# Performance work log

Measured on AMD Instinct MI355X. Metric: run time of the kernel, lower is better.

## Reference

```python
import jax, jax.numpy as jnp
import numpy as np
import math

B, NP, PL, CIN = 32, 1024, 16, 8
C = PL * CIN          # channels = 128
D = 512               # d_model
H = 8                 # n_heads
DH = D // H           # 64
DFF = 2048
E, TOPK = 4, 2
M = int(DH * math.log(DH))  # 266 performer random features


def _ortho_proj(m, d, rng):
    # gaussian-orthogonal random features, rows rescaled by gaussian norms (FAVOR+, scaling=0)
    blocks = []
    for _ in range(m // d + 1):
        q, _ = np.linalg.qr(rng.normal(size=(d, d)))
        blocks.append(q.T)
    mat = np.concatenate(blocks, 0)[:m]
    mult = np.linalg.norm(rng.normal(size=(m, d)), axis=1)
    return jnp.asarray((mat * mult[:, None]).astype(np.float32))


def setup_inputs() -> dict:
    key = jax.random.key(0)
    ks = jax.random.split(key, 16)
    rng = np.random.default_rng(0)
    s = lambda k, sh, fan: (jax.random.normal(k, sh, jnp.float32) / np.sqrt(fan))
    return {
        "x": jax.random.normal(ks[0], (B, NP, PL, CIN), jnp.float32),
        "emb_w": s(ks[1], (D, C), C),
        "wq": s(ks[2], (D, D), D), "bq": jnp.zeros((D,), jnp.float32),
        "wk": s(ks[3], (D, D), D), "bk": jnp.zeros((D,), jnp.float32),
        "wv": s(ks[4], (D, D), D), "bv": jnp.zeros((D,), jnp.float32),
        "wo": s(ks[5], (D, D), D), "bo": jnp.zeros((D,), jnp.float32),
        "proj": _ortho_proj(M, DH, rng),
        "ln2_g": jnp.ones((D,), jnp.float32), "ln2_b": jnp.zeros((D,), jnp.float32),
        "ln3_g": jnp.ones((D,), jnp.float32), "ln3_b": jnp.zeros((D,), jnp.float32),
        "gate_w": s(ks[6], (E, D), D), "gate_b": jnp.zeros((E,), jnp.float32),
        "w1": s(ks[7], (E, D, DFF), D), "b1": jnp.zeros((E, DFF), jnp.float32),
        "w2": s(ks[8], (E, DFF, D), DFF), "b2": jnp.zeros((E, D), jnp.float32),
    }


def _ln(x, g, b):
    mu = jnp.mean(x, -1, keepdims=True)
    var = jnp.var(x, -1, keepdims=True)
    return (x - mu) / jnp.sqrt(var + 1e-5) * g + b


def _phi(data, proj, is_query):
    # FAVOR+ softmax kernel feature map
    dh = data.shape[-1]
    m = proj.shape[0]
    dn = dh ** -0.25
    dash = jnp.einsum('...nd,md->...nm', data * dn, proj)
    diag = jnp.sum(jnp.square(data), -1, keepdims=True) * (0.5 * dn * dn)
    stab = jnp.max(dash, -1, keepdims=True) if is_query else jnp.max(dash)
    return (m ** -0.5) * (jnp.exp(dash - diag - stab) + 1e-4)


def reference(x, emb_w, wq, bq, wk, bk, wv, bv, wo, bo, proj,
              ln2_g, ln2_b, ln3_g, ln3_b, gate_w, gate_b, w1, b1, w2, b2):
    b, n = x.shape[0], x.shape[1]
    xe = x.reshape(b, n, -1) @ emb_w.T          # [b, n, D] (bias-free embedding)
    xe = xe[:, None]                            # [b, 1, n, D]
    # ---- Performer self-attention ----
    heads = lambda t: t.reshape(b, 1, n, H, DH).transpose(0, 1, 3, 2, 4)  # [b,1,h,n,dh]
    q = heads(xe @ wq.T + bq)
    k = heads(xe @ wk.T + bk)
    v = heads(xe @ wv.T + bv)
    qp = _phi(q, proj, True)                    # [b,1,h,n,m]
    kp = _phi(k, proj, False)
    ctx = jnp.einsum('...nm,...nd->...md', kp, v)           # [b,1,h,m,dh]
    den = jnp.einsum('...nm,...m->...n', qp, kp.sum(-2))    # [b,1,h,n]
    attn = jnp.einsum('...nm,...md->...nd', qp, ctx) / den[..., None]
    attn = attn.transpose(0, 1, 3, 2, 4).reshape(b, 1, n, D) @ wo.T + bo
    h1 = _ln(xe + attn, ln2_g, ln2_b)
    # ---- SparseMoE feed-forward (top-2 of 4 experts) ----
    t = h1.reshape(-1, D)                       # [T, D], T = b*n
    logits = t @ gate_w.T + gate_b              # [T, E]
    topv, topi = jax.lax.top_k(logits, TOPK)
    gwt = jax.nn.softmax(topv, -1)              # softmax over selected experts
    wfull = (jax.nn.one_hot(topi, E, dtype=t.dtype) * gwt[..., None]).sum(1)  # [T, E]
    hmid = jax.nn.relu(jnp.einsum('td,edf->etf', t, w1) + b1[:, None])        # [E, T, DFF]
    y = jnp.einsum('etf,efd->etd', hmid, w2) + b2[:, None]                    # [E, T, D]
    moe = jnp.einsum('te,etd->td', wfull, y).reshape(b, 1, n, D)
    return _ln(h1 + moe, ln3_g, ln3_b)          # dropout = identity in eval
```

## Files before the change

### kernel.cpp

```cpp
#include <hip/hip_runtime.h>
#include <math.h>

#define NBATCH 32
#define NPOS   1024
#define NTOK   32768
#define DMODEL 512
#define NHEAD  8
#define DHD    64
#define NROWS  262144
#define MMR    266
#define NDFF   2048
#define NEXP   4
#define CIN    128

#define DNSC   0.35355339059327373f
#define RSM    0.06131393394849658f
#define NEG_INF -3.0e38f

typedef _Float16 half8 __attribute__((ext_vector_type(8)));
typedef float    f32x4 __attribute__((ext_vector_type(4)));

static const size_t F_BUF1 = 0;
static const size_t F_CTX  = 16777216;
static const size_t F_KSUM = 21135360;
static const size_t F_PART = 21203456;
static const size_t F_STAB = 21205504;
static const size_t F_EFF  = 21205520;
static const size_t F_CNTI = 21402128;
static const size_t F_TOKI = 21402144;
static const size_t F_GWF  = 21533216;
static const size_t F_END  = 21664288;

__global__ __launch_bounds__(256) void fallback_zero_kernel(float* __restrict__ out) {
  out[(size_t)blockIdx.x * 256 + threadIdx.x] = 0.f;
}

__global__ __launch_bounds__(256) void zero_range_kernel(float* __restrict__ p, int n) {
  int i = blockIdx.x * 256 + threadIdx.x;
  if (i < n) p[i] = 0.f;
}

__global__ __launch_bounds__(128) void effmat_kernel(
    const float* __restrict__ wq, const float* __restrict__ wk, const float* __restrict__ wv,
    const float* __restrict__ emb, float* __restrict__ eff)
{
  __shared__ float wrow[512];
  const int bid = blockIdx.x;
  const int mat = bid >> 9;
  const int n   = bid & 511;
  const float* W = (mat == 0) ? wq : ((mat == 1) ? wk : wv);
  const int tid = threadIdx.x;
  for (int i = tid; i < 512; i += 128) wrow[i] = W[n * 512 + i];
  __syncthreads();
  float acc = 0.f;
  for (int d = 0; d < 512; ++d) acc += wrow[d] * emb[d * CIN + tid];
  eff[mat * 65536 + n * CIN + tid] = acc;
}

__device__ __forceinline__ void stage_proj(float* pj, const float* __restrict__ proj, int tid) {
  for (int idx = tid; idx < 272 * 68; idx += 256) pj[idx] = 0.f;
  __syncthreads();
  for (int idx = tid; idx < MMR * 64; idx += 256) {
    int m = idx >> 6, d = idx & 63;
    pj[m * 68 + d] = proj[idx];
  }
}

__global__ __launch_bounds__(256) void gemm_nt_kernel(
    const float* __restrict__ A, const float* __restrict__ W, int K,
    const float* __restrict__ A2, const float* __restrict__ W2, int K2,
    const float* __restrict__ bias, float* __restrict__ C, int N, int ncb)
{
  __shared__ float As[32][64];
  __shared__ float Ws[32][64];
  const int tid  = threadIdx.x;
  const int bx   = blockIdx.x % ncb;
  const int by   = blockIdx.x / ncb;
  const int row0 = by * 64, col0 = bx * 64;
  const int tx   = tid & 15, ty = tid >> 4;
  const int lr   = tid >> 3;
  const int lk   = (tid & 7) * 4;
  float acc[4][4] = {};
  for (int pass = 0; pass < 2; ++pass) {
    const float* Ap = pass ? A2 : A;
    const float* Wp = pass ? W2 : W;
    const int    Kp = pass ? K2 : K;
    if (!Ap) continue;
    for (int k0 = 0; k0 < Kp; k0 += 32) {
      __syncthreads();
#pragma unroll
      for (int rr = 0; rr < 2; ++rr) {
        const int r = lr + rr * 32;
        float4 a4 = *(const float4*)&Ap[(size_t)(row0 + r) * Kp + k0 + lk];
        As[lk + 0][r] = a4.x; As[lk + 1][r] = a4.y; As[lk + 2][r] = a4.z; As[lk + 3][r] = a4.w;
        float4 w4 = *(const float4*)&Wp[(size_t)(col0 + r) * Kp + k0 + lk];
        Ws[lk + 0][r] = w4.x; Ws[lk + 1][r] = w4.y; Ws[lk + 2][r] = w4.z; Ws[lk + 3][r] = w4.w;
      }
      __syncthreads();
#pragma unroll
      for (int kk = 0; kk < 32; ++kk) {
        float4 av = *(const float4*)&As[kk][ty * 4];
        float4 wv = *(const float4*)&Ws[kk][tx * 4];
        acc[0][0] += av.x * wv.x; acc[0][1] += av.x * wv.y; acc[0][2] += av.x * wv.z; acc[0][3] += av.x * wv.w;
        acc[1][0] += av.y * wv.x; acc[1][1] += av.y * wv.y; acc[1][2] += av.y * wv.z; acc[1][3] += av.y * wv.w;
        acc[2][0] += av.z * wv.x; acc[2][1] += av.z * wv.y; acc[2][2] += av.z * wv.z; acc[2][3] += av.z * wv.w;
        acc[3][0] += av.w * wv.x; acc[3][1] += av.w * wv.y; acc[3][2] += av.w * wv.z; acc[3][3] += av.w * wv.w;
      }
    }
  }
#pragma unroll
  for (int i = 0; i < 4; ++i) {
    const int row = row0 + ty * 4 + i;
    const int col = col0 + tx * 4;
    float4 o = make_float4(acc[i][0], acc[i][1], acc[i][2], acc[i][3]);
    if (bias) {
      float4 b4 = *(const float4*)&bias[col];
      o.x += b4.x; o.y += b4.y; o.z += b4.z; o.w += b4.w;
    }
    *(float4*)&C[(size_t)row * N + col] = o;
  }
}

__global__ __launch_bounds__(256) void kdash_max_kernel(
    const float* __restrict__ Kbuf, const float* __restrict__ proj, float* __restrict__ partial)
{
  __shared__ float pj[272 * 68];
  __shared__ float kl[32 * 68];
  __shared__ float red[256];
  const int tid = threadIdx.x;
  stage_proj(pj, proj, tid);
  const int i8 = tid >> 3, ml = tid & 7, mb = ml * 34;
  const size_t rid0 = (size_t)blockIdx.x * 128;
  float mx = NEG_INF;
  for (int ch = 0; ch < 4; ++ch) {
    __syncthreads();
    for (int idx = tid; idx < 2048; idx += 256) {
      int r = idx >> 6, dd = idx & 63;
      kl[r * 68 + dd] = Kbuf[(rid0 + ch * 32 + r) * 64 + dd] * DNSC;
    }
    __syncthreads();
    float dacc[34];
#pragma unroll
    for (int j = 0; j < 34; ++j) dacc[j] = 0.f;
    for (int d0 = 0; d0 < 64; d0 += 4) {
      float4 k4 = *(const float4*)&kl[i8 * 68 + d0];
#pragma unroll
      for (int j = 0; j < 34; ++j) {
        float4 p4 = *(const float4*)&pj[(mb + j) * 68 + d0];
        dacc[j] += k4.x * p4.x + k4.y * p4.y + k4.z * p4.z + k4.w * p4.w;
      }
    }
#pragma unroll
    for (int j = 0; j < 34; ++j) {
      int m = mb + j;
      mx = fmaxf(mx, (m < MMR) ? dacc[j] : NEG_INF);
    }
  }
  red[tid] = mx;
  __syncthreads();
  for (int st = 128; st > 0; st >>= 1) {
    if (tid < st) red[tid] = fmaxf(red[tid], red[tid + st]);
    __syncthreads();
  }
  if (tid == 0) partial[blockIdx.x] = red[0];
}

__global__ __launch_bounds__(256) void reduce_max_kernel(
    const float* __restrict__ part, float* __restrict__ stab, int n)
{
  __shared__ float red[256];
  float m = NEG_INF;
  for (int i = threadIdx.x; i < n; i += 256) m = fmaxf(m, part[i]);
  red[threadIdx.x] = m;
  __syncthreads();
  for (int st = 128; st > 0; st >>= 1) {
    if (threadIdx.x < st) red[threadIdx.x] = fmaxf(red[threadIdx.x], red[threadIdx.x + st]);
    __syncthreads();
  }
  if (threadIdx.x == 0) stab[0] = red[0];
}

__global__ __launch_bounds__(256) void ctx_kernel(
    const float* __restrict__ Kbuf, const float* __restrict__ Vbuf,
    const float* __restrict__ proj, const float* __restrict__ stabp,
    float* __restrict__ ctxg, float* __restrict__ ksumg)
{
  __shared__ float pj[272 * 68];
  __shared__ float kl[32 * 68];
  __shared__ float vl[32 * 68];
  __shared__ float kp[32 * 272];
  __shared__ float ks[272];
  const int tid = threadIdx.x;
  const int bh = blockIdx.x & 255;
  const int chunk = blockIdx.x >> 8;
  const int b = bh >> 3, h = bh & 7;
  const float stab = stabp[0];
  stage_proj(pj, proj, tid);
  for (int m = tid; m < 272; m += 256) ks[m] = 0.f;
  const int d = tid & 63, mg = tid >> 6;
  const int i8 = tid >> 3, ml = tid & 7, mb = ml * 34;
  float acc[68];
#pragma unroll
  for (int jj = 0; jj < 68; ++jj) acc[jj] = 0.f;
  for (int n0 = chunk * 256; n0 < chunk * 256 + 256; n0 += 32) {
    __syncthreads();
    for (int idx = tid; idx < 2048; idx += 256) {
      int r = idx >> 6, dd = idx & 63;
      size_t g = ((size_t)(b * NPOS + n0 + r)) * DMODEL + h * DHD + dd;
      kl[r * 68 + dd] = Kbuf[g] * DNSC;
      vl[r * 68 + dd] = Vbuf[g];
    }
    __syncthreads();
    float dacc[34];
#pragma unroll
    for (int j = 0; j < 34; ++j) dacc[j] = 0.f;
    float diag = 0.f;
    for (int d0 = 0; d0 < 64; d0 += 4) {
      float4 k4 = *(const float4*)&kl[i8 * 68 + d0];
      diag += k4.x * k4.x + k4.y * k4.y + k4.z * k4.z + k4.w * k4.w;
#pragma unroll
      for (int j = 0; j < 34; ++j) {
        float4 p4 = *(const float4*)&pj[(mb + j) * 68 + d0];
        dacc[j] += k4.x * p4.x + k4.y * p4.y + k4.z * p4.z + k4.w * p4.w;
      }
    }
    diag *= 0.5f;
#pragma unroll
    for (int j = 0; j < 34; ++j) {
      int m = mb + j;
      if (m < MMR) kp[i8 * 272 + m] = RSM * (expf(dacc[j] - diag - stab) + 1e-4f);
    }
    if (ml < 6) kp[i8 * 272 + MMR + ml] = 0.f;
    __syncthreads();
    for (int m = tid; m < MMR; m += 256) {
      float s = 0.f;
#pragma unroll 8
      for (int i = 0; i < 32; ++i) s += kp[i * 272 + m];
      ks[m] += s;
    }
    for (int i = 0; i < 32; ++i) {
      const float vv = vl[i * 68 + d];
      const float* kr = &kp[i * 272 + mg * 68];
#pragma unroll
      for (int jj = 0; jj < 17; ++jj) {
        float4 k4 = *(const float4*)&kr[jj * 4];
        acc[4 * jj + 0] += k4.x * vv;
        acc[4 * jj + 1] += k4.y * vv;
        acc[4 * jj + 2] += k4.z * vv;
        acc[4 * jj + 3] += k4.w * vv;
      }
    }
  }
  const size_t cb = (size_t)bh * MMR * DHD;
#pragma unroll
  for (int jj = 0; jj < 68; ++jj) {
    int m = mg * 68 + jj;
    if (m < MMR) atomicAdd(&ctxg[cb + (size_t)m * 64 + d], acc[jj]);
  }
  for (int m = tid; m < MMR; m += 256) atomicAdd(&ksumg[bh * MMR + m], ks[m]);
}

__global__ __launch_bounds__(256) void attn_kernel(
    const float* __restrict__ Qbuf, const float* __restrict__ ctxg,
    const float* __restrict__ ksumg, const float* __restrict__ proj,
    float* __restrict__ attnb)
{
  __shared__ float pj[272 * 68];
  __shared__ float ql[32 * 68];
  __shared__ float qp[32 * 272];
  __shared__ float ks[272];
  __shared__ float den_s[32];
  const int tid = threadIdx.x;
  const int bh = blockIdx.x >> 5;
  const int nc = blockIdx.x & 31;
  const int b = bh >> 3, h = bh & 7;
  const int n0 = nc * 32;
  stage_proj(pj, proj, tid);
  for (int m = tid; m < 272; m += 256) ks[m] = (m < MMR) ? ksumg[bh * MMR + m] : 0.f;
  for (int idx = tid; idx < 2048; idx += 256) {
    int r = idx >> 6, dd = idx & 63;
    ql[r * 68 + dd] = Qbuf[((size_t)(b * NPOS + n0 + r)) * DMODEL + h * DHD + dd] * DNSC;
  }
  __syncthreads();
  const int i8 = tid >> 3, ml = tid & 7, mb = ml * 34;
  float dacc[34];
#pragma unroll
  for (int j = 0; j < 34; ++j) dacc[j] = 0.f;
  float diag = 0.f;
  for (int d0 = 0; d0 < 64; d0 += 4) {
    float4 k4 = *(const float4*)&ql[i8 * 68 + d0];
    diag += k4.x * k4.x + k4.y * k4.y + k4.z * k4.z + k4.w * k4.w;
#pragma unroll
    for (int j = 0; j < 34; ++j) {
      float4 p4 = *(const float4*)&pj[(mb + j) * 68 + d0];
      dacc[j] += k4.x * p4.x + k4.y * p4.y + k4.z * p4.z + k4.w * p4.w;
    }
  }
  diag *= 0.5f;
  float mx = NEG_INF;
#pragma unroll
  for (int j = 0; j < 34; ++j) {
    int m = mb + j;
    mx = fmaxf(mx, (m < MMR) ? dacc[j] : NEG_INF);
  }
#pragma unroll
  for (int off = 1; off < 8; off <<= 1) mx = fmaxf(mx, __shfl_xor(mx, off));
  float dp = 0.f;
#pragma unroll
  for (int j = 0; j < 34; ++j) {
    int m = mb + j;
    if (m < MMR) {
      float v = RSM * (expf(dacc[j] - diag - mx) + 1e-4f);
      qp[i8 * 272 + m] = v;
      dp += v * ks[m];
    }
  }
  if (ml < 6) qp[i8 * 272 + MMR + ml] = 0.f;
#pragma unroll
  for (int off = 1; off < 8; off <<= 1) dp += __shfl_xor(dp, off);
  if (ml == 0) den_s[i8] = dp;
  __syncthreads();
  const int lane = tid & 63, wid = tid >> 6;
  float acc[8];
#pragma unroll
  for (int t = 0; t < 8; ++t) acc[t] = 0.f;
  const float* cb = ctxg + (size_t)bh * MMR * DHD + lane;
  for (int m0 = 0; m0 < 264; m0 += 4) {
    float c0 = cb[(size_t)(m0 + 0) * 64];
    float c1 = cb[(size_t)(m0 + 1) * 64];
    float c2 = cb[(size_t)(m0 + 2) * 64];
    float c3 = cb[(size_t)(m0 + 3) * 64];
#pragma unroll
    for (int t = 0; t < 8; ++t) {
      float4 q4 = *(const float4*)&qp[(wid + 4 * t) * 272 + m0];
      acc[t] += q4.x * c0 + q4.y * c1 + q4.z * c2 + q4.w * c3;
    }
  }
  {
    float c0 = cb[264 * 64], c1 = cb[265 * 64];
#pragma unroll
    for (int t = 0; t < 8; ++t)
      acc[t] += qp[(wid + 4 * t) * 272 + 264] * c0 + qp[(wid + 4 * t) * 272 + 265] * c1;
  }
#pragma unroll
  for (int t = 0; t < 8; ++t) {
    int r = wid + 4 * t;
    size_t o = ((size_t)(b * NPOS + n0 + r)) * DMODEL + h * DHD + lane;
    attnb[o] = acc[t] / den_s[r];
  }
}

__global__ __launch_bounds__(256) void ln_kernel(
    const float* __restrict__ in, const float* __restrict__ g, const float* __restrict__ bb,
    float* __restrict__ out, float* __restrict__ out2)
{
  const int row = blockIdx.x, tid = threadIdx.x;
  float2 x = *(const float2*)&in[(size_t)row * DMODEL + tid * 2];
  float s = x.x + x.y, sq = x.x * x.x + x.y * x.y;
#pragma unroll
  for (int off = 32; off > 0; off >>= 1) {
    s += __shfl_down(s, off);
    sq += __shfl_down(sq, off);
  }
  __shared__ float ps[4], pq[4];
  __shared__ float smu, srv;
  const int wv = tid >> 6, ln = tid & 63;
  if (ln == 0) { ps[wv] = s; pq[wv] = sq; }
  __syncthreads();
  if (tid == 0) {
    float S = ps[0] + ps[1] + ps[2] + ps[3];
    float Q = pq[0] + pq[1] + pq[2] + pq[3];
    float mu = S / 512.f;
    float var = Q / 512.f - mu * mu;
    smu = mu;
    srv = 1.0f / sqrtf(var + 1e-5f);
  }
  __syncthreads();
  const float mu = smu, rv = srv;
  const int c = tid * 2;
  float y0 = (x.x - mu) * rv * g[c] + bb[c];
  float y1 = (x.y - mu) * rv * g[c + 1] + bb[c + 1];
  out[(size_t)row * DMODEL + c] = y0;
  out[(size_t)row * DMODEL + c + 1] = y1;
  if (out2) {
    out2[(size_t)row * DMODEL + c] = y0;
    out2[(size_t)row * DMODEL + c + 1] = y1;
  }
}

__global__ __launch_bounds__(64) void zero_cnt_kernel(int* __restrict__ cnt)
{
  if (threadIdx.x < NEXP) cnt[threadIdx.x] = 0;
}

__global__ __launch_bounds__(256) void gate_kernel(
    const float* __restrict__ h1, const float* __restrict__ gw, const float* __restrict__ gb,
    int* __restrict__ cnt, int* __restrict__ toks, float* __restrict__ gws)
{
  const int wv = threadIdx.x >> 6, ln = threadIdx.x & 63;
  const int tok = blockIdx.x * 4 + wv;
  const float* hr = h1 + (size_t)tok * DMODEL;
  float p0 = 0, p1 = 0, p2 = 0, p3 = 0;
#pragma unroll
  for (int k = 0; k < 8; ++k) {
    float xv = hr[ln + 64 * k];
    p0 += xv * gw[0 * DMODEL + ln + 64 * k];
    p1 += xv * gw[1 * DMODEL + ln + 64 * k];
    p2 += xv * gw[2 * DMODEL + ln + 64 * k];
    p3 += xv * gw[3 * DMODEL + ln + 64 * k];
  }
#pragma unroll
  for (int off = 32; off > 0; off >>= 1) {
    p0 += __shfl_down(p0, off);
    p1 += __shfl_down(p1, off);
    p2 += __shfl_down(p2, off);
    p3 += __shfl_down(p3, off);
  }
  if (ln == 0) {
    p0 += gb[0]; p1 += gb[1]; p2 += gb[2]; p3 += gb[3];
    int i0 = 0; float v0 = p0;
    if (p1 > v0) { v0 = p1; i0 = 1; }
    if (p2 > v0) { v0 = p2; i0 = 2; }
    if (p3 > v0) { v0 = p3; i0 = 3; }
    int i1 = -1; float v1 = NEG_INF;
    if (i0 != 0 && p0 > v1) { v1 = p0; i1 = 0; }
    if (i0 != 1 && p1 > v1) { v1 = p1; i1 = 1; }
    if (i0 != 2 && p2 > v1) { v1 = p2; i1 = 2; }
    if (i0 != 3 && p3 > v1) { v1 = p3; i1 = 3; }
    float e = expf(v1 - v0);
    float w0 = 1.f / (1.f + e);
    float w1 = e / (1.f + e);
    int pos0 = atomicAdd(&cnt[i0], 1);
    toks[i0 * NTOK + pos0] = tok;
    gws[i0 * NTOK + pos0] = w0;
    int pos1 = atomicAdd(&cnt[i1], 1);
    toks[i1 * NTOK + pos1] = tok;
    gws[i1 * NTOK + pos1] = w1;
  }
}

__global__ __launch_bounds__(256) void transpose_f16_kernel(
    const float* __restrict__ in, _Float16* __restrict__ outp, int R, int C)
{
  __shared__ float tl[32][33];
  const int bid = blockIdx.x;
  const int e  = bid >> 10;
  const int t2 = bid & 1023;
  const int tC = C >> 5;
  const int r0 = (t2 / tC) << 5;
  const int c0 = (t2 % tC) << 5;
  const float* ine  = in   + (size_t)e * R * C;
  _Float16*    oute = outp + (size_t)e * R * C;
  const int ci = threadIdx.x & 31, ri = threadIdx.x >> 5;
#pragma unroll
  for (int i = 0; i < 4; ++i)
    tl[ri + i * 8][ci] = ine[(size_t)(r0 + ri + i * 8) * C + c0 + ci];
  __syncthreads();
  const int rr = threadIdx.x & 31, cc = threadIdx.x >> 5;
#pragma unroll
  for (int i = 0; i < 4; ++i)
    oute[(size_t)(c0 + cc + i * 8) * R + r0 + rr] = (_Float16)tl[rr][cc + i * 8];
}

__global__ __launch_bounds__(512) void moe_mfma_kernel(
    const float* __restrict__ h1, const _Float16* __restrict__ w1t, const float* __restrict__ b1,
    const _Float16* __restrict__ w2t, const float* __restrict__ b2,
    const int* __restrict__ cnt, const int* __restrict__ toks, const float* __restrict__ gws,
    float* __restrict__ Z)
{
  __shared__ _Float16 t_lds[64 * 520];
  __shared__ _Float16 hm[64 * 264];
  __shared__ int   tk_s[64];
  __shared__ float gw_s[64];
  const int tid = threadIdx.x;
  const int e = blockIdx.x >> 10;
  const int tile = blockIdx.x & 1023;
  const int cn = cnt[e];
  if (tile * 64 >= cn) return;
  if (tid < 64) {
    int idx = tile * 64 + tid;
    if (idx < cn) { tk_s[tid] = toks[e * NTOK + idx]; gw_s[tid] = gws[e * NTOK + idx]; }
    else          { tk_s[tid] = -1;                   gw_s[tid] = 0.f; }
  }
  __syncthreads();
  for (int it = tid; it < 64 * 128; it += 512) {
    int r = it >> 7, c4 = (it & 127) * 4;
    int tk = tk_s[r];
    float4 v = make_float4(0.f, 0.f, 0.f, 0.f);
    if (tk >= 0) v = *(const float4*)&h1[(size_t)tk * DMODEL + c4];
    _Float16* p = &t_lds[r * 520 + c4];
    p[0] = (_Float16)v.x; p[1] = (_Float16)v.y; p[2] = (_Float16)v.z; p[3] = (_Float16)v.w;
  }
  __syncthreads();

  const int w = tid >> 6, l = tid & 63;
  const int lr = l & 15, lg = l >> 4;
  const _Float16* w1e = w1t + (size_t)e * NDFF * DMODEL;
  const _Float16* w2e = w2t + (size_t)e * DMODEL * NDFF;
  const float* b1e = b1 + e * NDFF;

  f32x4 acc2[4][4];
#pragma unroll
  for (int mt = 0; mt < 4; ++mt)
#pragma unroll
    for (int nt = 0; nt < 4; ++nt) acc2[mt][nt] = (f32x4){0.f, 0.f, 0.f, 0.f};

  for (int fc = 0; fc < 8; ++fc) {
    f32x4 acc1[4][2];
#pragma unroll
    for (int mt = 0; mt < 4; ++mt)
#pragma unroll
      for (int nt1 = 0; nt1 < 2; ++nt1) acc1[mt][nt1] = (f32x4){0.f, 0.f, 0.f, 0.f};
#pragma unroll
    for (int ks = 0; ks < 16; ++ks) {
      half8 am[4];
#pragma unroll
      for (int mt = 0; mt < 4; ++mt)
        am[mt] = *(const half8*)&t_lds[(mt * 16 + lr) * 520 + ks * 32 + lg * 8];
#pragma unroll
      for (int nt1 = 0; nt1 < 2; ++nt1) {
        half8 bfr = *(const half8*)&w1e[(size_t)(fc * 256 + w * 32 + nt1 * 16 + lr) * DMODEL + ks * 32 + lg * 8];
#pragma unroll
        for (int mt = 0; mt < 4; ++mt)
          acc1[mt][nt1] = __builtin_amdgcn_mfma_f32_16x16x32_f16(am[mt], bfr, acc1[mt][nt1], 0, 0, 0);
      }
    }
#pragma unroll
    for (int nt1 = 0; nt1 < 2; ++nt1) {
      float b1v = b1e[fc * 256 + w * 32 + nt1 * 16 + lr];
#pragma unroll
      for (int mt = 0; mt < 4; ++mt)
#pragma unroll
        for (int r = 0; r < 4; ++r)
          hm[(mt * 16 + lg * 4 + r) * 264 + w * 32 + nt1 * 16 + lr] =
              (_Float16)fmaxf(acc1[mt][nt1][r] + b1v, 0.f);
    }
    __syncthreads();
#pragma unroll
    for (int ks2 = 0; ks2 < 8; ++ks2) {
      half8 am[4];
#pragma unroll
      for (int mt = 0; mt < 4; ++mt)
        am[mt] = *(const half8*)&hm[(mt * 16 + lr) * 264 + ks2 * 32 + lg * 8];
#pragma unroll
      for (int nt = 0; nt < 4; ++nt) {
        half8 bfr = *(const half8*)&w2e[(size_t)(w * 64 + nt * 16 + lr) * NDFF + fc * 256 + ks2 * 32 + lg * 8];
#pragma unroll
        for (int mt = 0; mt < 4; ++mt)
          acc2[mt][nt] = __builtin_amdgcn_mfma_f32_16x16x32_f16(am[mt], bfr, acc2[mt][nt], 0, 0, 0);
      }
    }
    __syncthreads();
  }

  const float* b2e = b2 + e * DMODEL;
#pragma unroll
  for (int nt = 0; nt < 4; ++nt) {
    float b2v = b2e[w * 64 + nt * 16 + lr];
#pragma unroll
    for (int mt = 0; mt < 4; ++mt) {
#pragma unroll
      for (int r = 0; r < 4; ++r) {
        int row = mt * 16 + lg * 4 + r;
        int tk = tk_s[row];
        if (tk >= 0)
          atomicAdd(&Z[(size_t)tk * DMODEL + w * 64 + nt * 16 + lr],
                    (acc2[mt][nt][r] + b2v) * gw_s[row]);
      }
    }
  }
}

extern "C" void kernel_launch(void* const* d_in, const int* in_sizes, int n_in,
                              void* d_out, int out_size, void* d_ws, size_t ws_size,
                              hipStream_t stream) {
  const float* x     = (const float*)d_in[0];
  const float* emb_w = (const float*)d_in[1];
  const float* wq    = (const float*)d_in[2];
  const float* bq    = (const float*)d_in[3];
  const float* wk    = (const float*)d_in[4];
  const float* bk    = (const float*)d_in[5];
  const float* wv    = (const float*)d_in[6];
  const float* bv    = (const float*)d_in[7];
  const float* wo    = (const float*)d_in[8];
  const float* bo    = (const float*)d_in[9];
  const float* proj  = (const float*)d_in[10];
  const float* ln2g  = (const float*)d_in[11];
  const float* ln2b  = (const float*)d_in[12];
  const float* ln3g  = (const float*)d_in[13];
  const float* ln3b  = (const float*)d_in[14];
  const float* gatew = (const float*)d_in[15];
  const float* gateb = (const float*)d_in[16];
  const float* w1    = (const float*)d_in[17];
  const float* b1    = (const float*)d_in[18];
  const float* w2    = (const float*)d_in[19];
  const float* b2    = (const float*)d_in[20];
  float* out = (float*)d_out;
  float* ws  = (float*)d_ws;

  if (ws_size < F_END * sizeof(float)) {
    fallback_zero_kernel<<<NTOK * 2, 256, 0, stream>>>(out);
    return;
  }

  float* BUF1 = ws + F_BUF1;
  float* BUF2 = out;
  int*   cnt  = (int*)(ws + F_CNTI);
  int*   toks = (int*)(ws + F_TOKI);
  float* gwf  = ws + F_GWF;
  _Float16* w1t = (_Float16*)(ws + F_CTX);
  _Float16* w2t = w1t + (size_t)NEXP * NDFF * DMODEL;

  zero_cnt_kernel<<<1, 64, 0, stream>>>(cnt);
  zero_range_kernel<<<17292, 256, 0, stream>>>(ws + F_CTX, 4358144 + 68096);
  effmat_kernel<<<1536, 128, 0, stream>>>(wq, wk, wv, emb_w, ws + F_EFF);
  gemm_nt_kernel<<<4096, 256, 0, stream>>>(x, ws + F_EFF + 65536, CIN, nullptr, nullptr, 0, bk, BUF1, DMODEL, 8);
  gemm_nt_kernel<<<4096, 256, 0, stream>>>(x, ws + F_EFF + 131072, CIN, nullptr, nullptr, 0, bv, BUF2, DMODEL, 8);
  kdash_max_kernel<<<2048, 256, 0, stream>>>(BUF1, proj, ws + F_PART);
  reduce_max_kernel<<<1, 256, 0, stream>>>(ws + F_PART, ws + F_STAB, 2048);
  ctx_kernel<<<1024, 256, 0, stream>>>(BUF1, BUF2, proj, ws + F_STAB, ws + F_CTX, ws + F_KSUM);
  gemm_nt_kernel<<<4096, 256, 0, stream>>>(x, ws + F_EFF, CIN, nullptr, nullptr, 0, bq, BUF1, DMODEL, 8);
  attn_kernel<<<8192, 256, 0, stream>>>(BUF1, ws + F_CTX, ws + F_KSUM, proj, BUF2);
  transpose_f16_kernel<<<4096, 256, 0, stream>>>(w1, w1t, DMODEL, NDFF);
  transpose_f16_kernel<<<4096, 256, 0, stream>>>(w2, w2t, NDFF, DMODEL);
  gemm_nt_kernel<<<4096, 256, 0, stream>>>(BUF2, wo, DMODEL, x, emb_w, CIN, bo, BUF1, DMODEL, 8);
  ln_kernel<<<NTOK, 256, 0, stream>>>(BUF1, ln2g, ln2b, BUF2, BUF1);
  gate_kernel<<<8192, 256, 0, stream>>>(BUF2, gatew, gateb, cnt, toks, gwf);
  moe_mfma_kernel<<<4096, 512, 0, stream>>>(BUF2, w1t, b1, w2t, b2, cnt, toks, gwf, BUF1);
  ln_kernel<<<NTOK, 256, 0, stream>>>(BUF1, ln3g, ln3b, out, nullptr);
}
```

Measured before the change: 4.495 ms.

## Restructure performer feature kernels with packed proj layout and wider blocks

Adds a one-time pack of the random-feature projection into a d-major, 17-feature-grouped layout. The k-max, ctx and attention kernels now run as 1024-thread blocks that split the 64-dim dot product across lane quarters and reduce with shuffles. The ctx kernel now uses one block per batch-head over the full sequence and writes its results directly, which removes the global atomics and the workspace zeroing kernel. Feature values kp/qp are stored in LDS as fp16 to cut shared-memory footprint and bandwidth, at some cost in precision. Fewer ctx blocks (256) may reduce occupancy, and LDS use per block grows.

```diff
diff --git a/kernel.cpp b/kernel.cpp
--- a/kernel.cpp
+++ b/kernel.cpp
@@ -18,6 +18,7 @@
 #define NEG_INF -3.0e38f
 
 typedef _Float16 half8 __attribute__((ext_vector_type(8)));
+typedef _Float16 half4 __attribute__((ext_vector_type(4)));
 typedef float    f32x4 __attribute__((ext_vector_type(4)));
 
 static const size_t F_BUF1 = 0;
@@ -29,15 +30,29 @@
 static const size_t F_CNTI = 21402128;
 static const size_t F_TOKI = 21402144;
 static const size_t F_GWF  = 21533216;
-static const size_t F_END  = 21664288;
+static const size_t F_PJT  = 21664288;
+static const size_t F_END  = 21684768;
+
+#define DASH17(da, q) \
+  da[0]+=q*pA.x; da[1]+=q*pA.y; da[2]+=q*pA.z; da[3]+=q*pA.w; \
+  da[4]+=q*pB.x; da[5]+=q*pB.y; da[6]+=q*pB.z; da[7]+=q*pB.w; \
+  da[8]+=q*pC.x; da[9]+=q*pC.y; da[10]+=q*pC.z; da[11]+=q*pC.w; \
+  da[12]+=q*pD.x; da[13]+=q*pD.y; da[14]+=q*pD.z; da[15]+=q*pD.w; \
+  da[16]+=q*pE;
 
 __global__ __launch_bounds__(256) void fallback_zero_kernel(float* __restrict__ out) {
   out[(size_t)blockIdx.x * 256 + threadIdx.x] = 0.f;
 }
 
-__global__ __launch_bounds__(256) void zero_range_kernel(float* __restrict__ p, int n) {
-  int i = blockIdx.x * 256 + threadIdx.x;
-  if (i < n) p[i] = 0.f;
+__global__ __launch_bounds__(256) void proj_pack_kernel(
+    const float* __restrict__ proj, float* __restrict__ projT)
+{
+  int idx = blockIdx.x * 256 + threadIdx.x;
+  if (idx >= 20480) return;
+  int d = idx / 320, rem = idx % 320;
+  int g = rem / 20, j = rem % 20;
+  int m = g * 17 + j;
+  projT[idx] = (j < 17 && m < MMR) ? proj[m * 64 + d] : 0.f;
 }
 
 __global__ __launch_bounds__(128) void effmat_kernel(
@@ -55,15 +70,6 @@
   float acc = 0.f;
   for (int d = 0; d < 512; ++d) acc += wrow[d] * emb[d * CIN + tid];
   eff[mat * 65536 + n * CIN + tid] = acc;
-}
-
-__device__ __forceinline__ void stage_proj(float* pj, const float* __restrict__ proj, int tid) {
-  for (int idx = tid; idx < 272 * 68; idx += 256) pj[idx] = 0.f;
-  __syncthreads();
-  for (int idx = tid; idx < MMR * 64; idx += 256) {
-    int m = idx >> 6, d = idx & 63;
-    pj[m * 68 + d] = proj[idx];
-  }
 }
 
 __global__ __launch_bounds__(256) void gemm_nt_kernel(
@@ -121,44 +127,53 @@
   }
 }
 
-__global__ __launch_bounds__(256) void kdash_max_kernel(
-    const float* __restrict__ Kbuf, const float* __restrict__ proj, float* __restrict__ partial)
-{
-  __shared__ float pj[272 * 68];
+__global__ __launch_bounds__(1024) void kdash_max_kernel(
+    const float* __restrict__ Kbuf, const float* __restrict__ projT, float* __restrict__ partial)
+{
+  __shared__ float pjG[20480];
   __shared__ float kl[32 * 68];
-  __shared__ float red[256];
+  __shared__ float red[1024];
   const int tid = threadIdx.x;
-  stage_proj(pj, proj, tid);
-  const int i8 = tid >> 3, ml = tid & 7, mb = ml * 34;
-  const size_t rid0 = (size_t)blockIdx.x * 128;
-  float mx = NEG_INF;
-  for (int ch = 0; ch < 4; ++ch) {
-    __syncthreads();
-    for (int idx = tid; idx < 2048; idx += 256) {
+  for (int i = tid; i < 20480; i += 1024) pjG[i] = projT[i];
+  const int w = tid >> 6, l = tid & 63;
+  const int ml = l & 15, ds = l >> 4;
+  const int dbase = ds * 16;
+  const int r0 = 2 * w;
+  float mxl = NEG_INF;
+  for (int t = 0; t < 16; ++t) {
+    __syncthreads();
+    for (int idx = tid; idx < 2048; idx += 1024) {
       int r = idx >> 6, dd = idx & 63;
-      kl[r * 68 + dd] = Kbuf[(rid0 + ch * 32 + r) * 64 + dd] * DNSC;
-    }
-    __syncthreads();
-    float dacc[34];
-#pragma unroll
-    for (int j = 0; j < 34; ++j) dacc[j] = 0.f;
-    for (int d0 = 0; d0 < 64; d0 += 4) {
-      float4 k4 = *(const float4*)&kl[i8 * 68 + d0];
-#pragma unroll
-      for (int j = 0; j < 34; ++j) {
-        float4 p4 = *(const float4*)&pj[(mb + j) * 68 + d0];
-        dacc[j] += k4.x * p4.x + k4.y * p4.y + k4.z * p4.z + k4.w * p4.w;
-      }
-    }
-#pragma unroll
-    for (int j = 0; j < 34; ++j) {
-      int m = mb + j;
-      mx = fmaxf(mx, (m < MMR) ? dacc[j] : NEG_INF);
-    }
-  }
-  red[tid] = mx;
-  __syncthreads();
-  for (int st = 128; st > 0; st >>= 1) {
+      kl[r * 68 + dd] = Kbuf[((size_t)blockIdx.x * 512 + t * 32 + r) * 64 + dd] * DNSC;
+    }
+    __syncthreads();
+    float da0[17], da1[17];
+#pragma unroll
+    for (int j = 0; j < 17; ++j) { da0[j] = 0.f; da1[j] = 0.f; }
+    for (int dd = 0; dd < 16; ++dd) {
+      int d = dbase + dd;
+      float q0 = kl[r0 * 68 + d], q1 = kl[r0 * 68 + 68 + d];
+      const float* pr = &pjG[d * 320 + ml * 20];
+      float4 pA = *(const float4*)pr, pB = *(const float4*)(pr + 4),
+             pC = *(const float4*)(pr + 8), pD = *(const float4*)(pr + 12);
+      float pE = pr[16];
+      DASH17(da0, q0)
+      DASH17(da1, q1)
+    }
+#pragma unroll
+    for (int j = 0; j < 17; ++j) {
+      da0[j] += __shfl_xor(da0[j], 16); da0[j] += __shfl_xor(da0[j], 32);
+      da1[j] += __shfl_xor(da1[j], 16); da1[j] += __shfl_xor(da1[j], 32);
+    }
+#pragma unroll
+    for (int j = 0; j < 17; ++j) {
+      int m = ml * 17 + j;
+      if (m < MMR) { mxl = fmaxf(mxl, da0[j]); mxl = fmaxf(mxl, da1[j]); }
+    }
+  }
+  red[tid] = mxl;
+  __syncthreads();
+  for (int st = 512; st > 0; st >>= 1) {
     if (tid < st) red[tid] = fmaxf(red[tid], red[tid + st]);
     __syncthreads();
   }
@@ -180,173 +195,208 @@
   if (threadIdx.x == 0) stab[0] = red[0];
 }
 
-__global__ __launch_bounds__(256) void ctx_kernel(
+__global__ __launch_bounds__(1024) void ctx_kernel(
     const float* __restrict__ Kbuf, const float* __restrict__ Vbuf,
-    const float* __restrict__ proj, const float* __restrict__ stabp,
+    const float* __restrict__ projT, const float* __restrict__ stabp,
     float* __restrict__ ctxg, float* __restrict__ ksumg)
 {
-  __shared__ float pj[272 * 68];
+  __shared__ float pjG[20480];
   __shared__ float kl[32 * 68];
   __shared__ float vl[32 * 68];
-  __shared__ float kp[32 * 272];
+  __shared__ _Float16 kp16[32 * 320];
   __shared__ float ks[272];
   const int tid = threadIdx.x;
-  const int bh = blockIdx.x & 255;
-  const int chunk = blockIdx.x >> 8;
+  const int bh = blockIdx.x;
   const int b = bh >> 3, h = bh & 7;
   const float stab = stabp[0];
-  stage_proj(pj, proj, tid);
-  for (int m = tid; m < 272; m += 256) ks[m] = 0.f;
+  for (int i = tid; i < 20480; i += 1024) pjG[i] = projT[i];
+  if (tid < 272) ks[tid] = 0.f;
+  const int w = tid >> 6, l = tid & 63;
+  const int ml = l & 15, ds = l >> 4;
+  const int dbase = ds * 16;
+  const int r0 = 2 * w;
+  const int jh = ds >> 1, rsel = ds & 1;
   const int d = tid & 63, mg = tid >> 6;
-  const int i8 = tid >> 3, ml = tid & 7, mb = ml * 34;
-  float acc[68];
-#pragma unroll
-  for (int jj = 0; jj < 68; ++jj) acc[jj] = 0.f;
-  for (int n0 = chunk * 256; n0 < chunk * 256 + 256; n0 += 32) {
-    __syncthreads();
-    for (int idx = tid; idx < 2048; idx += 256) {
+  const int ksm = tid >> 1, ksih = tid & 1;
+  const int ksg = ksm / 17, ksj = ksm - ksg * 17;
+  float acc[17];
+#pragma unroll
+  for (int j = 0; j < 17; ++j) acc[j] = 0.f;
+
+  for (int t = 0; t < 32; ++t) {
+    __syncthreads();
+    for (int idx = tid; idx < 2048; idx += 1024) {
       int r = idx >> 6, dd = idx & 63;
-      size_t g = ((size_t)(b * NPOS + n0 + r)) * DMODEL + h * DHD + dd;
+      size_t g = ((size_t)(b * NPOS + t * 32 + r)) * DMODEL + h * DHD + dd;
       kl[r * 68 + dd] = Kbuf[g] * DNSC;
       vl[r * 68 + dd] = Vbuf[g];
     }
     __syncthreads();
-    float dacc[34];
-#pragma unroll
-    for (int j = 0; j < 34; ++j) dacc[j] = 0.f;
-    float diag = 0.f;
-    for (int d0 = 0; d0 < 64; d0 += 4) {
-      float4 k4 = *(const float4*)&kl[i8 * 68 + d0];
-      diag += k4.x * k4.x + k4.y * k4.y + k4.z * k4.z + k4.w * k4.w;
-#pragma unroll
-      for (int j = 0; j < 34; ++j) {
-        float4 p4 = *(const float4*)&pj[(mb + j) * 68 + d0];
-        dacc[j] += k4.x * p4.x + k4.y * p4.y + k4.z * p4.z + k4.w * p4.w;
+    float da0[17], da1[17]; float dg0 = 0.f, dg1 = 0.f;
+#pragma unroll
+    for (int j = 0; j < 17; ++j) { da0[j] = 0.f; da1[j] = 0.f; }
+    for (int dd = 0; dd < 16; ++dd) {
+      int dq = dbase + dd;
+      float q0 = kl[r0 * 68 + dq], q1 = kl[r0 * 68 + 68 + dq];
+      const float* pr = &pjG[dq * 320 + ml * 20];
+      float4 pA = *(const float4*)pr, pB = *(const float4*)(pr + 4),
+             pC = *(const float4*)(pr + 8), pD = *(const float4*)(pr + 12);
+      float pE = pr[16];
+      dg0 += q0 * q0; dg1 += q1 * q1;
+      DASH17(da0, q0)
+      DASH17(da1, q1)
+    }
+#pragma unroll
+    for (int j = 0; j < 17; ++j) {
+      da0[j] += __shfl_xor(da0[j], 16); da0[j] += __shfl_xor(da0[j], 32);
+      da1[j] += __shfl_xor(da1[j], 16); da1[j] += __shfl_xor(da1[j], 32);
+    }
+    dg0 += __shfl_xor(dg0, 16); dg0 += __shfl_xor(dg0, 32);
+    dg1 += __shfl_xor(dg1, 16); dg1 += __shfl_xor(dg1, 32);
+    float dgx = rsel ? dg1 : dg0;
+    const int irow = r0 + rsel;
+#pragma unroll
+    for (int k = 0; k < 9; ++k) {
+      int j = 2 * k + jh;
+      if (j < 17) {
+        int m = ml * 17 + j;
+        float dv = rsel ? da1[j] : da0[j];
+        float v = 0.f;
+        if (m < MMR) v = RSM * (expf(dv - 0.5f * dgx - stab) + 1e-4f);
+        kp16[irow * 320 + ml * 20 + j] = (_Float16)v;
       }
     }
-    diag *= 0.5f;
-#pragma unroll
-    for (int j = 0; j < 34; ++j) {
-      int m = mb + j;
-      if (m < MMR) kp[i8 * 272 + m] = RSM * (expf(dacc[j] - diag - stab) + 1e-4f);
-    }
-    if (ml < 6) kp[i8 * 272 + MMR + ml] = 0.f;
-    __syncthreads();
-    for (int m = tid; m < MMR; m += 256) {
+    __syncthreads();
+    if (tid < 544) {
       float s = 0.f;
-#pragma unroll 8
-      for (int i = 0; i < 32; ++i) s += kp[i * 272 + m];
-      ks[m] += s;
+      const _Float16* kb = &kp16[ksih * 16 * 320 + ksg * 20 + ksj];
+#pragma unroll
+      for (int i = 0; i < 16; ++i) s += (float)kb[i * 320];
+      s += __shfl_xor(s, 1);
+      if (ksih == 0) ks[ksm] += s;
     }
     for (int i = 0; i < 32; ++i) {
-      const float vv = vl[i * 68 + d];
-      const float* kr = &kp[i * 272 + mg * 68];
-#pragma unroll
-      for (int jj = 0; jj < 17; ++jj) {
-        float4 k4 = *(const float4*)&kr[jj * 4];
-        acc[4 * jj + 0] += k4.x * vv;
-        acc[4 * jj + 1] += k4.y * vv;
-        acc[4 * jj + 2] += k4.z * vv;
-        acc[4 * jj + 3] += k4.w * vv;
-      }
-    }
-  }
+      float vv = vl[i * 68 + d];
+      const _Float16* kr = &kp16[i * 320 + mg * 20];
+      half4 k0 = *(const half4*)kr;
+      half4 k1 = *(const half4*)(kr + 4);
+      half4 k2 = *(const half4*)(kr + 8);
+      half4 k3 = *(const half4*)(kr + 12);
+      float kE = (float)kr[16];
+      acc[0] += (float)k0.x * vv; acc[1] += (float)k0.y * vv; acc[2] += (float)k0.z * vv; acc[3] += (float)k0.w * vv;
+      acc[4] += (float)k1.x * vv; acc[5] += (float)k1.y * vv; acc[6] += (float)k1.z * vv; acc[7] += (float)k1.w * vv;
+      acc[8] += (float)k2.x * vv; acc[9] += (float)k2.y * vv; acc[10] += (float)k2.z * vv; acc[11] += (float)k2.w * vv;
+      acc[12] += (float)k3.x * vv; acc[13] += (float)k3.y * vv; acc[14] += (float)k3.z * vv; acc[15] += (float)k3.w * vv;
+      acc[16] += kE * vv;
+    }
+  }
+  __syncthreads();
   const size_t cb = (size_t)bh * MMR * DHD;
 #pragma unroll
-  for (int jj = 0; jj < 68; ++jj) {
-    int m = mg * 68 + jj;
-    if (m < MMR) atomicAdd(&ctxg[cb + (size_t)m * 64 + d], acc[jj]);
-  }
-  for (int m = tid; m < MMR; m += 256) atomicAdd(&ksumg[bh * MMR + m], ks[m]);
-}
-
-__global__ __launch_bounds__(256) void attn_kernel(
+  for (int j = 0; j < 17; ++j) {
+    int m = mg * 17 + j;
+    if (m < MMR) ctxg[cb + (size_t)m * 64 + d] = acc[j];
+  }
+  if (tid < MMR) ksumg[bh * MMR + tid] = ks[tid];
+}
+
+__global__ __launch_bounds__(1024) void attn_kernel(
     const float* __restrict__ Qbuf, const float* __restrict__ ctxg,
-    const float* __restrict__ ksumg, const float* __restrict__ proj,
+    const float* __restrict__ ksumg, const float* __restrict__ projT,
     float* __restrict__ attnb)
 {
-  __shared__ float pj[272 * 68];
-  __shared__ float ql[32 * 68];
-  __shared__ float qp[32 * 272];
+  __shared__ float pjG[20480];
+  __shared__ float ql[64 * 68];
+  __shared__ _Float16 qp16[64 * 272];
   __shared__ float ks[272];
-  __shared__ float den_s[32];
+  __shared__ float den_s[64];
   const int tid = threadIdx.x;
-  const int bh = blockIdx.x >> 5;
-  const int nc = blockIdx.x & 31;
+  const int bh = blockIdx.x >> 4;
+  const int n0 = (blockIdx.x & 15) * 64;
   const int b = bh >> 3, h = bh & 7;
-  const int n0 = nc * 32;
-  stage_proj(pj, proj, tid);
-  for (int m = tid; m < 272; m += 256) ks[m] = (m < MMR) ? ksumg[bh * MMR + m] : 0.f;
-  for (int idx = tid; idx < 2048; idx += 256) {
+  for (int i = tid; i < 20480; i += 1024) pjG[i] = projT[i];
+  if (tid < 272) ks[tid] = (tid < MMR) ? ksumg[bh * MMR + tid] : 0.f;
+  for (int idx = tid; idx < 4096; idx += 1024) {
     int r = idx >> 6, dd = idx & 63;
     ql[r * 68 + dd] = Qbuf[((size_t)(b * NPOS + n0 + r)) * DMODEL + h * DHD + dd] * DNSC;
   }
   __syncthreads();
-  const int i8 = tid >> 3, ml = tid & 7, mb = ml * 34;
-  float dacc[34];
-#pragma unroll
-  for (int j = 0; j < 34; ++j) dacc[j] = 0.f;
-  float diag = 0.f;
-  for (int d0 = 0; d0 < 64; d0 += 4) {
-    float4 k4 = *(const float4*)&ql[i8 * 68 + d0];
-    diag += k4.x * k4.x + k4.y * k4.y + k4.z * k4.z + k4.w * k4.w;
-#pragma unroll
-    for (int j = 0; j < 34; ++j) {
-      float4 p4 = *(const float4*)&pj[(mb + j) * 68 + d0];
-      dacc[j] += k4.x * p4.x + k4.y * p4.y + k4.z * p4.z + k4.w * p4.w;
-    }
-  }
-  diag *= 0.5f;
-  float mx = NEG_INF;
-#pragma unroll
-  for (int j = 0; j < 34; ++j) {
-    int m = mb + j;
-    mx = fmaxf(mx, (m < MMR) ? dacc[j] : NEG_INF);
-  }
-#pragma unroll
-  for (int off = 1; off < 8; off <<= 1) mx = fmaxf(mx, __shfl_xor(mx, off));
-  float dp = 0.f;
-#pragma unroll
-  for (int j = 0; j < 34; ++j) {
-    int m = mb + j;
-    if (m < MMR) {
-      float v = RSM * (expf(dacc[j] - diag - mx) + 1e-4f);
-      qp[i8 * 272 + m] = v;
-      dp += v * ks[m];
-    }
-  }
-  if (ml < 6) qp[i8 * 272 + MMR + ml] = 0.f;
-#pragma unroll
-  for (int off = 1; off < 8; off <<= 1) dp += __shfl_xor(dp, off);
-  if (ml == 0) den_s[i8] = dp;
-  __syncthreads();
-  const int lane = tid & 63, wid = tid >> 6;
-  float acc[8];
-#pragma unroll
-  for (int t = 0; t < 8; ++t) acc[t] = 0.f;
+  const int w = tid >> 6, l = tid & 63;
+  const int ml = l & 15, ds = l >> 4;
+  const int dbase = ds * 16;
+  const int jh = ds >> 1, rsel = ds & 1;
+  for (int s = 0; s < 2; ++s) {
+    const int r0 = s * 32 + 2 * w;
+    float da0[17], da1[17]; float dg0 = 0.f, dg1 = 0.f;
+#pragma unroll
+    for (int j = 0; j < 17; ++j) { da0[j] = 0.f; da1[j] = 0.f; }
+    for (int dd = 0; dd < 16; ++dd) {
+      int dq = dbase + dd;
+      float q0 = ql[r0 * 68 + dq], q1 = ql[r0 * 68 + 68 + dq];
+      const float* pr = &pjG[dq * 320 + ml * 20];
+      float4 pA = *(const float4*)pr, pB = *(const float4*)(pr + 4),
+             pC = *(const float4*)(pr + 8), pD = *(const float4*)(pr + 12);
+      float pE = pr[16];
+      dg0 += q0 * q0; dg1 += q1 * q1;
+      DASH17(da0, q0)
+      DASH17(da1, q1)
+    }
+#pragma unroll
+    for (int j = 0; j < 17; ++j) {
+      da0[j] += __shfl_xor(da0[j], 16); da0[j] += __shfl_xor(da0[j], 32);
+      da1[j] += __shfl_xor(da1[j], 16); da1[j] += __shfl_xor(da1[j], 32);
+    }
+    dg0 += __shfl_xor(dg0, 16); dg0 += __shfl_xor(dg0, 32);
+    dg1 += __shfl_xor(dg1, 16); dg1 += __shfl_xor(dg1, 32);
+    float mx0 = NEG_INF, mx1 = NEG_INF;
+#pragma unroll
+    for (int j = 0; j < 17; ++j) {
+      int m = ml * 17 + j;
+      if (m < MMR) { mx0 = fmaxf(mx0, da0[j]); mx1 = fmaxf(mx1, da1[j]); }
+    }
+#pragma unroll
+    for (int off = 1; off < 16; off <<= 1) {
+      mx0 = fmaxf(mx0, __shfl_xor(mx0, off));
+      mx1 = fmaxf(mx1, __shfl_xor(mx1, off));
+    }
+    float dgx = rsel ? dg1 : dg0;
+    float mxx = rsel ? mx1 : mx0;
+    const int row = r0 + rsel;
+    float dp = 0.f;
+#pragma unroll
+    for (int k = 0; k < 9; ++k) {
+      int j = 2 * k + jh;
+      if (j < 17) {
+        int m = ml * 17 + j;
+        float dv = rsel ? da1[j] : da0[j];
+        float v = 0.f;
+        if (m < MMR) { v = RSM * (expf(dv - 0.5f * dgx - mxx) + 1e-4f); dp += v * ks[m]; }
+        qp16[row * 272 + m] = (_Float16)v;
+      }
+    }
+    dp += __shfl_xor(dp, 1); dp += __shfl_xor(dp, 2); dp += __shfl_xor(dp, 4);
+    dp += __shfl_xor(dp, 8); dp += __shfl_xor(dp, 32);
+    if ((l & 47) == 0) den_s[row] = dp;
+  }
+  __syncthreads();
+  const int wg = tid >> 6, lane = tid & 63;
+  float acc[4] = {0.f, 0.f, 0.f, 0.f};
   const float* cb = ctxg + (size_t)bh * MMR * DHD + lane;
-  for (int m0 = 0; m0 < 264; m0 += 4) {
+  for (int m0 = 0; m0 < 272; m0 += 4) {
     float c0 = cb[(size_t)(m0 + 0) * 64];
     float c1 = cb[(size_t)(m0 + 1) * 64];
     float c2 = cb[(size_t)(m0 + 2) * 64];
     float c3 = cb[(size_t)(m0 + 3) * 64];
 #pragma unroll
-    for (int t = 0; t < 8; ++t) {
-      float4 q4 = *(const float4*)&qp[(wid + 4 * t) * 272 + m0];
-      acc[t] += q4.x * c0 + q4.y * c1 + q4.z * c2 + q4.w * c3;
-    }
-  }
-  {
-    float c0 = cb[264 * 64], c1 = cb[265 * 64];
-#pragma unroll
-    for (int t = 0; t < 8; ++t)
-      acc[t] += qp[(wid + 4 * t) * 272 + 264] * c0 + qp[(wid + 4 * t) * 272 + 265] * c1;
-  }
-#pragma unroll
-  for (int t = 0; t < 8; ++t) {
-    int r = wid + 4 * t;
-    size_t o = ((size_t)(b * NPOS + n0 + r)) * DMODEL + h * DHD + lane;
-    attnb[o] = acc[t] / den_s[r];
+    for (int tt = 0; tt < 4; ++tt) {
+      half4 q4 = *(const half4*)&qp16[(wg * 4 + tt) * 272 + m0];
+      acc[tt] += (float)q4.x * c0 + (float)q4.y * c1 + (float)q4.z * c2 + (float)q4.w * c3;
+    }
+  }
+#pragma unroll
+  for (int tt = 0; tt < 4; ++tt) {
+    int r = wg * 4 + tt;
+    attnb[((size_t)(b * NPOS + n0 + r)) * DMODEL + h * DHD + lane] = acc[tt] / den_s[r];
   }
 }
 
@@ -612,15 +662,15 @@
   _Float16* w2t = w1t + (size_t)NEXP * NDFF * DMODEL;
 
   zero_cnt_kernel<<<1, 64, 0, stream>>>(cnt);
-  zero_range_kernel<<<17292, 256, 0, stream>>>(ws + F_CTX, 4358144 + 68096);
+  proj_pack_kernel<<<80, 256, 0, stream>>>(proj, ws + F_PJT);
   effmat_kernel<<<1536, 128, 0, stream>>>(wq, wk, wv, emb_w, ws + F_EFF);
   gemm_nt_kernel<<<4096, 256, 0, stream>>>(x, ws + F_EFF + 65536, CIN, nullptr, nullptr, 0, bk, BUF1, DMODEL, 8);
   gemm_nt_kernel<<<4096, 256, 0, stream>>>(x, ws + F_EFF + 131072, CIN, nullptr, nullptr, 0, bv, BUF2, DMODEL, 8);
-  kdash_max_kernel<<<2048, 256, 0, stream>>>(BUF1, proj, ws + F_PART);
-  reduce_max_kernel<<<1, 256, 0, stream>>>(ws + F_PART, ws + F_STAB, 2048);
-  ctx_kernel<<<1024, 256, 0, stream>>>(BUF1, BUF2, proj, ws + F_STAB, ws + F_CTX, ws + F_KSUM);
+  kdash_max_kernel<<<512, 1024, 0, stream>>>(BUF1, ws + F_PJT, ws + F_PART);
+  reduce_max_kernel<<<1, 256, 0, stream>>>(ws + F_PART, ws + F_STAB, 512);
+  ctx_kernel<<<256, 1024, 0, stream>>>(BUF1, BUF2, ws + F_PJT, ws + F_STAB, ws + F_CTX, ws + F_KSUM);
   gemm_nt_kernel<<<4096, 256, 0, stream>>>(x, ws + F_EFF, CIN, nullptr, nullptr, 0, bq, BUF1, DMODEL, 8);
-  attn_kernel<<<8192, 256, 0, stream>>>(BUF1, ws + F_CTX, ws + F_KSUM, proj, BUF2);
+  attn_kernel<<<4096, 1024, 0, stream>>>(BUF1, ws + F_CTX, ws + F_KSUM, ws + F_PJT, BUF2);
   transpose_f16_kernel<<<4096, 256, 0, stream>>>(w1, w1t, DMODEL, NDFF);
   transpose_f16_kernel<<<4096, 256, 0, stream>>>(w2, w2t, NDFF, DMODEL);
   gemm_nt_kernel<<<4096, 256, 0, stream>>>(BUF2, wo, DMODEL, x, emb_w, CIN, bo, BUF1, DMODEL, 8);
```

Measured after the change: 5.262 ms. 17.1% more time.
